# Optimization experiments

Hardware: AMD Instinct MI355X
Metric: run time of the kernel (lower is better)

Reference implementation:

```python
import jax, jax.numpy as jnp
import numpy as np

N_NODES = 50000
N_EDGES = 600000
N_RELS = 19
D_IN = 128
D_HID = 64
D_OUT = 2


def setup_inputs() -> dict:
    key = jax.random.key(0)
    ks = jax.random.split(key, 10)
    feat = jax.random.normal(ks[0], (N_NODES, D_IN), dtype=jnp.float32)
    src = jax.random.randint(ks[1], (N_EDGES,), 0, N_NODES)
    dst = jax.random.randint(ks[2], (N_EDGES,), 0, N_NODES)
    etype = jax.random.randint(ks[3], (N_EDGES,), 0, N_RELS)
    s1 = 1.0 / np.sqrt(D_IN)
    s2 = 1.0 / np.sqrt(D_HID)
    W1 = jax.random.normal(ks[4], (N_RELS, D_IN, D_HID), dtype=jnp.float32) * s1
    loop1 = jax.random.normal(ks[5], (D_IN, D_HID), dtype=jnp.float32) * s1
    b1 = jnp.zeros((D_HID,), dtype=jnp.float32)
    W2 = jax.random.normal(ks[6], (N_RELS, D_HID, D_OUT), dtype=jnp.float32) * s2
    loop2 = jax.random.normal(ks[7], (D_HID, D_OUT), dtype=jnp.float32) * s2
    b2 = jnp.zeros((D_OUT,), dtype=jnp.float32)
    return {"feat": feat, "W1": W1, "loop1": loop1, "b1": b1,
            "W2": W2, "loop2": loop2, "b2": b2,
            "src": src, "dst": dst, "etype": etype}


def _rel_graph_conv(h, W, loop_w, bias, src, dst, etype, activation):
    # Per-relation transform of all nodes: [N, R, O]; then gather per edge.
    # (num_rels * out_feat is small, so this is cheaper than gathering W per edge.)
    transformed = jnp.einsum('nd,rdo->nro', h, W)
    msg = transformed[src, etype]                      # [E, O] edge messages
    agg = jax.ops.segment_sum(msg, dst, num_segments=h.shape[0])  # scatter-add
    out = agg + h @ loop_w + bias                      # self-loop + bias
    if activation is not None:
        out = activation(out)
    return out


def reference(feat, W1, loop1, b1, W2, loop2, b2, src, dst, etype):
    h = _rel_graph_conv(feat, W1, loop1, b1, src, dst, etype, jax.nn.relu)
    h = _rel_graph_conv(h, W2, loop2, b2, src, dst, etype, None)
    return h
```

## Files before the change

kernel.cpp:

```cpp
#include <hip/hip_runtime.h>

#define N_NODES 50000
#define N_EDGES 600000
#define N_RELS  19
#define D_IN    128
#define D_HID   64
#define D_OUT   2
#define BSH     9
#define NB      ((N_NODES + 511) >> 9)
#define NSEG    (NB * N_RELS)
#define SL_BLOCKS ((N_NODES + 63) / 64)
#define PREP_ELEMS (N_RELS * D_HID * D_IN + 64 * 64 + D_HID * D_IN)
#define PREP_BLOCKS ((PREP_ELEMS + 255) / 256)

typedef unsigned short u16;
typedef unsigned int   u32;
typedef __attribute__((ext_vector_type(8))) short sfrag;
typedef __attribute__((ext_vector_type(4))) float f32x4;

__device__ __forceinline__ u16 f2bf(float f){
  union { float f; u32 i; } v; v.f = f;
  u32 r = v.i + 0x7fffu + ((v.i >> 16) & 1u);
  return (u16)(r >> 16);
}
__device__ __forceinline__ float bf2f(u16 u){
  union { u32 i; float f; } v; v.i = ((u32)u) << 16; return v.f;
}
__device__ __forceinline__ u32 pack2(float lo, float hi){
  return (u32)f2bf(lo) | ((u32)f2bf(hi) << 16);
}

__global__ __launch_bounds__(256) void k_pre(const float* __restrict__ feat,
                                             u16* __restrict__ featb,
                                             const int* __restrict__ src,
                                             const int* __restrict__ et,
                                             const int* __restrict__ dst,
                                             int* __restrict__ seg_hist,
                                             int* __restrict__ hist_dst){
  int i = blockIdx.x * 256 + threadIdx.x;
  float4 f = ((const float4*)feat)[i];
  uint2 p; p.x = pack2(f.x, f.y); p.y = pack2(f.z, f.w);
  ((uint2*)featb)[i] = p;
  if (i < N_EDGES) {
    int key = (src[i] >> BSH) * N_RELS + et[i];
    atomicAdd(&seg_hist[key * 16], 1);
    atomicAdd(&hist_dst[dst[i]], 1);
  }
}

__global__ __launch_bounds__(256) void k_prep(
    const int* __restrict__ hist_dst, int* __restrict__ dstart,
    int* __restrict__ cur_dst, int* __restrict__ gcnt,
    const int* __restrict__ seg_hist, int* __restrict__ seg_off,
    int* __restrict__ cur_seg,
    const float* __restrict__ W1, const float* __restrict__ loop1,
    const float* __restrict__ W2, const float* __restrict__ loop2,
    u16* __restrict__ W1Tb, u16* __restrict__ loop1Tb,
    u16* __restrict__ W2allT){
  if (blockIdx.x >= 197) {
    int idx = (blockIdx.x - 197) * 256 + threadIdx.x;
    const int T1  = N_RELS * D_HID * D_IN;
    const int T2c = T1 + 64 * 64;
    const int T3  = T2c + D_HID * D_IN;
    if (idx < T1) {
      int r = idx / (D_HID * D_IN);
      int t = idx - r * (D_HID * D_IN);
      int j = t >> 7, d = t & 127;
      W1Tb[idx] = f2bf(W1[(r * D_IN + d) * D_HID + j]);
    } else if (idx < T2c) {
      int k2 = idx - T1;
      int j = k2 >> 6, k = k2 & 63;
      float val = 0.f;
      if (j < N_RELS * D_OUT)      val = W2[((j >> 1) * D_HID + k) * D_OUT + (j & 1)];
      else if (j == 38)            val = loop2[k * 2];
      else if (j == 39)            val = loop2[k * 2 + 1];
      W2allT[k2] = f2bf(val);
    } else if (idx < T3) {
      int k2 = idx - T2c;
      int j = k2 >> 7, d = k2 & 127;
      loop1Tb[k2] = f2bf(loop1[d * D_HID + j]);
    }
    return;
  }
  if (blockIdx.x == 196) {
    __shared__ int ps[256];
    int tid = threadIdx.x;
    const int PER = (NSEG + 255) / 256;
    int lo = tid * PER, hi = lo + PER; if (hi > NSEG) hi = NSEG; if (lo > NSEG) lo = NSEG;
    int s = 0;
    for (int i = lo; i < hi; ++i) s += seg_hist[i * 16];
    ps[tid] = s;
    __syncthreads();
    if (tid == 0) { int a = 0; for (int j = 0; j < 256; ++j) { int x = ps[j]; ps[j] = a; a += x; } }
    __syncthreads();
    int eo = ps[tid];
    for (int i = lo; i < hi; ++i) {
      int c = seg_hist[i * 16];
      seg_off[i] = eo; cur_seg[i * 16] = eo;
      eo += c;
    }
    if (hi == NSEG) seg_off[NSEG] = eo;
    return;
  }
  __shared__ int wbase[4];
  int tid = threadIdx.x, lane = tid & 63, wv = tid >> 6;
  int n = blockIdx.x * 256 + tid;
  int v = (n < N_NODES) ? hist_dst[n] : 0;
  int x = v;
  #pragma unroll
  for (int o = 1; o < 64; o <<= 1) { int u = __shfl_up(x, o); if (lane >= o) x += u; }
  if (lane == 63) wbase[wv] = atomicAdd(gcnt, x);
  __syncthreads();
  int start = wbase[wv] + x - v;
  if (n < N_NODES) { dstart[n] = start; cur_dst[n] = start; }
}

__global__ __launch_bounds__(256) void k_scatter(const int* __restrict__ src,
                                                 const int* __restrict__ et,
                                                 int* __restrict__ cur_seg,
                                                 int* __restrict__ perm){
  int e = blockIdx.x * 256 + threadIdx.x;
  if (e >= N_EDGES) return;
  int key = (src[e] >> BSH) * N_RELS + et[e];
  int p = atomicAdd(&cur_seg[key * 16], 1);
  perm[p] = e;
}

__global__ __launch_bounds__(256, 4) void k_se1(
    const u16* __restrict__ featb, const u16* __restrict__ W1Tb,
    const u16* __restrict__ loop1Tb, const float* __restrict__ b1,
    const int* __restrict__ src, const int* __restrict__ dst,
    const int* __restrict__ perm, const int* __restrict__ seg_off,
    int* __restrict__ cur_dst, int* __restrict__ srel,
    u16* __restrict__ msgbuf, u16* __restrict__ agg1b){
  __shared__ __align__(16) u16 Bls[64][136];
  __shared__ __align__(16) u16 msg[128][72];
  __shared__ int posIds[128];
  int tid = threadIdx.x, lane = tid & 63, w4 = tid >> 6;
  int r16 = lane & 15, c4 = lane >> 4;

  if (blockIdx.x >= NSEG) {
    int base = (blockIdx.x - NSEG) * 64;
    { int j = tid >> 2, sg = tid & 3;
      const uint4* g = (const uint4*)(loop1Tb + j * 128) + sg * 4;
      uint4* d = (uint4*)&Bls[j][sg * 32];
      d[0] = g[0]; d[1] = g[1]; d[2] = g[2]; d[3] = g[3]; }
    int arow = base + w4 * 16 + r16; if (arow >= N_NODES) arow = N_NODES - 1;
    sfrag aF[4];
    #pragma unroll
    for (int kk = 0; kk < 4; ++kk)
      aF[kk] = *(const sfrag*)(featb + (size_t)arow * D_IN + kk * 32 + c4 * 8);
    __syncthreads();
    #pragma unroll
    for (int ct = 0; ct < 4; ++ct) {
      int col = ct * 16 + r16;
      f32x4 acc = {0.f, 0.f, 0.f, 0.f};
      #pragma unroll
      for (int kk = 0; kk < 4; ++kk) {
        sfrag bF = *(const sfrag*)&Bls[ct * 16 + r16][kk * 32 + c4 * 8];
        acc = __builtin_amdgcn_mfma_f32_16x16x32_bf16(aF[kk], bF, acc, 0, 0, 0);
      }
      float bias = b1[col];
      #pragma unroll
      for (int reg = 0; reg < 4; ++reg) {
        float v = acc[reg] + bias;
        float o = __shfl_xor(v, 1);
        if (!(lane & 1))
          *(u32*)&msg[w4 * 16 + c4 * 4 + reg][col] = pack2(v, o);
      }
    }
    { int j = lane >> 2, q = lane & 3;
      int n = base + w4 * 16 + j;
      if (n < N_NODES) {
        const uint4* mr = (const uint4*)&msg[w4 * 16 + j][q * 16];
        uint4* d = (uint4*)(agg1b + (size_t)n * D_HID + q * 16);
        d[0] = mr[0]; d[1] = mr[1];
      } }
    return;
  }

  const int q8 = NSEG >> 3, r8 = NSEG & 7;
  int xcd = blockIdx.x & 7, cidx = blockIdx.x >> 3;
  int seg = (xcd < r8 ? xcd * (q8 + 1) : r8 * (q8 + 1) + (xcd - r8) * q8) + cidx;
  int ts = seg_off[seg], c = seg_off[seg + 1] - ts;
  if (c == 0) return;
  int rel = seg - (seg / N_RELS) * N_RELS;

  {
    int j = tid >> 2, sg = tid & 3;
    const uint4* g = (const uint4*)(W1Tb + ((size_t)rel * 64 + j) * 128) + sg * 4;
    uint4* d = (uint4*)&Bls[j][sg * 32];
    d[0] = g[0]; d[1] = g[1]; d[2] = g[2]; d[3] = g[3];
  }
  __syncthreads();

  for (int t0 = 0; t0 < c; t0 += 128) {
    int vc = c - t0; if (vc > 128) vc = 128;
    int myPos = -1;
    if (tid < 128 && tid < vc) {
      int e = perm[ts + t0 + tid];
      myPos = atomicAdd(&cur_dst[dst[e]], 1);
      srel[myPos] = (src[e] << 5) | rel;
    }
    sfrag aF[2][4];
    #pragma unroll
    for (int mt = 0; mt < 2; ++mt) {
      int row = w4 * 32 + mt * 16 + r16;
      int rr = row < vc ? row : vc - 1;
      int s = src[perm[ts + t0 + rr]];
      const u16* ap = featb + (size_t)s * D_IN + c4 * 8;
      #pragma unroll
      for (int kk = 0; kk < 4; ++kk)
        aF[mt][kk] = *(const sfrag*)(ap + kk * 32);
    }
    #pragma unroll
    for (int ct = 0; ct < 4; ++ct) {
      sfrag bF[4];
      #pragma unroll
      for (int kk = 0; kk < 4; ++kk)
        bF[kk] = *(const sfrag*)&Bls[ct * 16 + r16][kk * 32 + c4 * 8];
      #pragma unroll
      for (int mt = 0; mt < 2; ++mt) {
        f32x4 acc = {0.f, 0.f, 0.f, 0.f};
        #pragma unroll
        for (int kk = 0; kk < 4; ++kk)
          acc = __builtin_amdgcn_mfma_f32_16x16x32_bf16(aF[mt][kk], bF[kk], acc, 0, 0, 0);
        #pragma unroll
        for (int reg = 0; reg < 4; ++reg) {
          float v = acc[reg];
          float o = __shfl_xor(v, 1);
          if (!(lane & 1)) {
            int orow = w4 * 32 + mt * 16 + c4 * 4 + reg;
            *(u32*)&msg[orow][ct * 16 + r16] = pack2(v, o);
          }
        }
      }
    }
    if (tid < 128) posIds[tid] = myPos;
    __syncthreads();
    { int row = tid >> 1, half = tid & 1;
      int pos = posIds[row];
      if (pos >= 0) {
        const uint4* mr = (const uint4*)&msg[row][half * 32];
        uint4* d = (uint4*)(msgbuf + (size_t)pos * D_HID + half * 32);
        d[0] = mr[0]; d[1] = mr[1]; d[2] = mr[2]; d[3] = mr[3];
      } }
    __syncthreads();
  }
}

__global__ __launch_bounds__(256) void k_agg(
    const u16* __restrict__ msgbuf, const int* __restrict__ dstart,
    const int* __restrict__ cnt, const u16* __restrict__ agg1b,
    const u16* __restrict__ W2allT, const float* __restrict__ b2,
    float* __restrict__ T2f, float* __restrict__ out){
  __shared__ u16   W2ls[64][66];
  __shared__ float h1s[4][68];
  int tid = threadIdx.x, wv = tid >> 6, lane = tid & 63;
  for (int i = tid; i < 64 * 64; i += 256) W2ls[i >> 6][i & 63] = W2allT[i];
  int n = blockIdx.x * 4 + wv;
  int s = dstart[n], epos = s + cnt[n];
  int h = lane >> 5, cc = lane & 31;
  float a0 = 0.f, a1 = 0.f;
  for (int i = s + h; i < epos; i += 2) {
    u32 v = ((const u32*)msgbuf)[(size_t)i * 32 + cc];
    a0 += bf2f((u16)(v & 0xffffu));
    a1 += bf2f((u16)(v >> 16));
  }
  a0 += __shfl_down(a0, 32);
  a1 += __shfl_down(a1, 32);
  if (h == 0) {
    u32 sv = ((const u32*)agg1b)[(size_t)n * 32 + cc];
    float v0 = a0 + bf2f((u16)(sv & 0xffffu));
    float v1 = a1 + bf2f((u16)(sv >> 16));
    v0 = v0 > 0.f ? v0 : 0.f;
    v1 = v1 > 0.f ? v1 : 0.f;
    h1s[wv][2 * cc]     = v0;
    h1s[wv][2 * cc + 1] = v1;
  }
  __syncthreads();
  if (lane < 40) {
    float acc = 0.f;
    #pragma unroll 8
    for (int k = 0; k < 64; ++k)
      acc += bf2f(W2ls[lane][k]) * h1s[wv][k];
    if (lane < 38) T2f[(size_t)n * 40 + lane] = acc;
    else           out[n * 2 + (lane - 38)] = acc + b2[lane - 38];
  }
}

__global__ __launch_bounds__(256) void k_fin(
    const float* __restrict__ T2f, const int* __restrict__ srel,
    const int* __restrict__ dstart, const int* __restrict__ cnt,
    float* __restrict__ out){
  int wv = threadIdx.x >> 6, lane = threadIdx.x & 63;
  int n = blockIdx.x * 4 + wv;
  int s = dstart[n], c = cnt[n];
  float ax = 0.f, ay = 0.f;
  for (int i = lane; i < c; i += 64) {
    int sr = srel[s + i];
    const float* p = T2f + (size_t)(sr >> 5) * 40 + (sr & 31) * 2;
    ax += p[0]; ay += p[1];
  }
  #pragma unroll
  for (int off = 32; off; off >>= 1) {
    ax += __shfl_down(ax, off);
    ay += __shfl_down(ay, off);
  }
  if (lane == 0) {
    out[n * 2]     += ax;
    out[n * 2 + 1] += ay;
  }
}

extern "C" void kernel_launch(void* const* d_in, const int* in_sizes, int n_in,
                              void* d_out, int out_size, void* d_ws, size_t ws_size,
                              hipStream_t stream){
  const float* feat  = (const float*)d_in[0];
  const float* W1    = (const float*)d_in[1];
  const float* loop1 = (const float*)d_in[2];
  const float* b1    = (const float*)d_in[3];
  const float* W2    = (const float*)d_in[4];
  const float* loop2 = (const float*)d_in[5];
  const float* b2    = (const float*)d_in[6];
  const int* src     = (const int*)d_in[7];
  const int* dst     = (const int*)d_in[8];
  const int* et      = (const int*)d_in[9];
  float* out = (float*)d_out;

  char* w = (char*)d_ws;
  u16*   W1Tb     = (u16*)(w);
  u16*   W2allT   = (u16*)(w + 311296);
  u16*   loop1Tb  = (u16*)(w + 319488);
  int*   seg_hist = (int*)(w + 335872);
  int*   gcnt     = (int*)(w + 455040);
  int*   hist_dst = (int*)(w + 455104);
  int*   seg_off  = (int*)(w + 655104);
  int*   cur_seg  = (int*)(w + 662592);
  int*   dstart   = (int*)(w + 781760);
  int*   cur_dst  = (int*)(w + 981760);
  int*   perm     = (int*)(w + 1181760);
  int*   srel     = (int*)(w + 3581760);
  u16*   featb    = (u16*)(w + 5981760);
  float* T2f      = (float*)(w + 5981760);
  u16*   agg1b    = (u16*)(w + 18781760);
  u16*   msgbuf   = (u16*)(w + 25181760);

  hipMemsetAsync(w + 335872, 0, 319232, stream);
  k_pre     <<<6250, 256, 0, stream>>>(feat, featb, src, et, dst, seg_hist, hist_dst);
  k_prep    <<<197 + PREP_BLOCKS, 256, 0, stream>>>(
                hist_dst, dstart, cur_dst, gcnt, seg_hist, seg_off, cur_seg,
                W1, loop1, W2, loop2, W1Tb, loop1Tb, W2allT);
  k_scatter <<<2344, 256, 0, stream>>>(src, et, cur_seg, perm);
  k_se1     <<<NSEG + SL_BLOCKS, 256, 0, stream>>>(
                featb, W1Tb, loop1Tb, b1, src, dst, perm, seg_off,
                cur_dst, srel, msgbuf, agg1b);
  k_agg     <<<12500, 256, 0, stream>>>(msgbuf, dstart, hist_dst, agg1b,
                                        W2allT, b2, T2f, out);
  k_fin     <<<12500, 256, 0, stream>>>(T2f, srel, dstart, hist_dst, out);
}
```

Before: 311.2 us.

## Split edge segments into fixed 128-edge tiles and make final layer edge-parallel atomics

The prep kernel now computes a tile list (segment id and start offset per 128-edge chunk), and the layer-1 message kernel launches one block per tile instead of one block per (node-bucket, relation) segment that looped over its chunks. This is meant to balance load across blocks and expose more parallelism. The final layer-2 aggregation switches from a per-destination-node wave reduction over CSR to an edge-parallel kernel that reads (src,rel,dst) pairs in segment order and does float atomicAdds into the output. The atomic version adds contention and a nondeterministic summation order, and the grid is oversized so many blocks exit early.

```diff
diff --git a/kernel.cpp b/kernel.cpp
--- a/kernel.cpp
+++ b/kernel.cpp
@@ -9,6 +9,7 @@
 #define BSH     9
 #define NB      ((N_NODES + 511) >> 9)
 #define NSEG    (NB * N_RELS)
+#define NTILE_CAP (NSEG + (N_EDGES + 127) / 128)
 #define SL_BLOCKS ((N_NODES + 63) / 64)
 #define PREP_ELEMS (N_RELS * D_HID * D_IN + 64 * 64 + D_HID * D_IN)
 #define PREP_BLOCKS ((PREP_ELEMS + 255) / 256)
@@ -52,7 +53,8 @@
     const int* __restrict__ hist_dst, int* __restrict__ dstart,
     int* __restrict__ cur_dst, int* __restrict__ gcnt,
     const int* __restrict__ seg_hist, int* __restrict__ seg_off,
-    int* __restrict__ cur_seg,
+    int* __restrict__ cur_seg, int* __restrict__ ntile,
+    int* __restrict__ tseg, int* __restrict__ tstart,
     const float* __restrict__ W1, const float* __restrict__ loop1,
     const float* __restrict__ W2, const float* __restrict__ loop2,
     u16* __restrict__ W1Tb, u16* __restrict__ loop1Tb,
@@ -83,21 +85,27 @@
     return;
   }
   if (blockIdx.x == 196) {
-    __shared__ int ps[256];
+    __shared__ int se_s[256], st_s[256];
     int tid = threadIdx.x;
     const int PER = (NSEG + 255) / 256;
     int lo = tid * PER, hi = lo + PER; if (hi > NSEG) hi = NSEG; if (lo > NSEG) lo = NSEG;
-    int s = 0;
-    for (int i = lo; i < hi; ++i) s += seg_hist[i * 16];
-    ps[tid] = s;
+    int se = 0, st = 0;
+    for (int i = lo; i < hi; ++i) { int c = seg_hist[i * 16]; se += c; st += (c + 127) >> 7; }
+    se_s[tid] = se; st_s[tid] = st;
     __syncthreads();
-    if (tid == 0) { int a = 0; for (int j = 0; j < 256; ++j) { int x = ps[j]; ps[j] = a; a += x; } }
+    if (tid == 0) {
+      int a = 0, b = 0;
+      for (int j = 0; j < 256; ++j) { int x = se_s[j], y = st_s[j]; se_s[j] = a; st_s[j] = b; a += x; b += y; }
+      ntile[0] = b;
+    }
     __syncthreads();
-    int eo = ps[tid];
+    int eo = se_s[tid], to = st_s[tid];
     for (int i = lo; i < hi; ++i) {
       int c = seg_hist[i * 16];
       seg_off[i] = eo; cur_seg[i * 16] = eo;
-      eo += c;
+      int nt = (c + 127) >> 7;
+      for (int k = 0; k < nt; ++k) { tseg[to + k] = i; tstart[to + k] = eo + (k << 7); }
+      eo += c; to += nt;
     }
     if (hi == NSEG) seg_off[NSEG] = eo;
     return;
@@ -131,16 +139,18 @@
     const u16* __restrict__ loop1Tb, const float* __restrict__ b1,
     const int* __restrict__ src, const int* __restrict__ dst,
     const int* __restrict__ perm, const int* __restrict__ seg_off,
-    int* __restrict__ cur_dst, int* __restrict__ srel,
-    u16* __restrict__ msgbuf, u16* __restrict__ agg1b){
+    const int* __restrict__ ntile_p, const int* __restrict__ tseg,
+    const int* __restrict__ tstart, int* __restrict__ cur_dst,
+    int2* __restrict__ sd2, u16* __restrict__ msgbuf,
+    u16* __restrict__ agg1b){
   __shared__ __align__(16) u16 Bls[64][136];
   __shared__ __align__(16) u16 msg[128][72];
   __shared__ int posIds[128];
   int tid = threadIdx.x, lane = tid & 63, w4 = tid >> 6;
   int r16 = lane & 15, c4 = lane >> 4;
 
-  if (blockIdx.x >= NSEG) {
-    int base = (blockIdx.x - NSEG) * 64;
+  if (blockIdx.x >= NTILE_CAP) {
+    int base = (blockIdx.x - NTILE_CAP) * 64;
     { int j = tid >> 2, sg = tid & 3;
       const uint4* g = (const uint4*)(loop1Tb + j * 128) + sg * 4;
       uint4* d = (uint4*)&Bls[j][sg * 32];
@@ -179,11 +189,16 @@
     return;
   }
 
-  const int q8 = NSEG >> 3, r8 = NSEG & 7;
-  int xcd = blockIdx.x & 7, cidx = blockIdx.x >> 3;
-  int seg = (xcd < r8 ? xcd * (q8 + 1) : r8 * (q8 + 1) + (xcd - r8) * q8) + cidx;
-  int ts = seg_off[seg], c = seg_off[seg + 1] - ts;
-  if (c == 0) return;
+  int nt = *ntile_p;
+  int pb = blockIdx.x;
+  if (pb >= nt) return;
+  int q8 = nt >> 3, r8 = nt & 7;
+  int xcd = pb & 7, cidx = pb >> 3;
+  int b = (xcd < r8 ? xcd * (q8 + 1) : r8 * (q8 + 1) + (xcd - r8) * q8) + cidx;
+
+  int seg = tseg[b];
+  int ts  = tstart[b];
+  int vc  = seg_off[seg + 1] - ts; if (vc > 128) vc = 128;
   int rel = seg - (seg / N_RELS) * N_RELS;
 
   {
@@ -192,61 +207,57 @@
     uint4* d = (uint4*)&Bls[j][sg * 32];
     d[0] = g[0]; d[1] = g[1]; d[2] = g[2]; d[3] = g[3];
   }
+  int myPos = -1;
+  if (tid < 128 && tid < vc) {
+    int e = perm[ts + tid];
+    int s2 = src[e], d2 = dst[e];
+    myPos = atomicAdd(&cur_dst[d2], 1);
+    sd2[ts + tid] = make_int2((s2 << 5) | rel, d2);
+  }
+  sfrag aF[2][4];
+  #pragma unroll
+  for (int mt = 0; mt < 2; ++mt) {
+    int row = w4 * 32 + mt * 16 + r16;
+    int rr = row < vc ? row : vc - 1;
+    int s = src[perm[ts + rr]];
+    const u16* ap = featb + (size_t)s * D_IN + c4 * 8;
+    #pragma unroll
+    for (int kk = 0; kk < 4; ++kk)
+      aF[mt][kk] = *(const sfrag*)(ap + kk * 32);
+  }
   __syncthreads();
-
-  for (int t0 = 0; t0 < c; t0 += 128) {
-    int vc = c - t0; if (vc > 128) vc = 128;
-    int myPos = -1;
-    if (tid < 128 && tid < vc) {
-      int e = perm[ts + t0 + tid];
-      myPos = atomicAdd(&cur_dst[dst[e]], 1);
-      srel[myPos] = (src[e] << 5) | rel;
-    }
-    sfrag aF[2][4];
+  #pragma unroll
+  for (int ct = 0; ct < 4; ++ct) {
+    sfrag bF[4];
+    #pragma unroll
+    for (int kk = 0; kk < 4; ++kk)
+      bF[kk] = *(const sfrag*)&Bls[ct * 16 + r16][kk * 32 + c4 * 8];
     #pragma unroll
     for (int mt = 0; mt < 2; ++mt) {
-      int row = w4 * 32 + mt * 16 + r16;
-      int rr = row < vc ? row : vc - 1;
-      int s = src[perm[ts + t0 + rr]];
-      const u16* ap = featb + (size_t)s * D_IN + c4 * 8;
+      f32x4 acc = {0.f, 0.f, 0.f, 0.f};
       #pragma unroll
       for (int kk = 0; kk < 4; ++kk)
-        aF[mt][kk] = *(const sfrag*)(ap + kk * 32);
-    }
-    #pragma unroll
-    for (int ct = 0; ct < 4; ++ct) {
-      sfrag bF[4];
+        acc = __builtin_amdgcn_mfma_f32_16x16x32_bf16(aF[mt][kk], bF[kk], acc, 0, 0, 0);
       #pragma unroll
-      for (int kk = 0; kk < 4; ++kk)
-        bF[kk] = *(const sfrag*)&Bls[ct * 16 + r16][kk * 32 + c4 * 8];
-      #pragma unroll
-      for (int mt = 0; mt < 2; ++mt) {
-        f32x4 acc = {0.f, 0.f, 0.f, 0.f};
-        #pragma unroll
-        for (int kk = 0; kk < 4; ++kk)
-          acc = __builtin_amdgcn_mfma_f32_16x16x32_bf16(aF[mt][kk], bF[kk], acc, 0, 0, 0);
-        #pragma unroll
-        for (int reg = 0; reg < 4; ++reg) {
-          float v = acc[reg];
-          float o = __shfl_xor(v, 1);
-          if (!(lane & 1)) {
-            int orow = w4 * 32 + mt * 16 + c4 * 4 + reg;
-            *(u32*)&msg[orow][ct * 16 + r16] = pack2(v, o);
-          }
+      for (int reg = 0; reg < 4; ++reg) {
+        float v = acc[reg];
+        float o = __shfl_xor(v, 1);
+        if (!(lane & 1)) {
+          int orow = w4 * 32 + mt * 16 + c4 * 4 + reg;
+          *(u32*)&msg[orow][ct * 16 + r16] = pack2(v, o);
         }
       }
     }
-    if (tid < 128) posIds[tid] = myPos;
-    __syncthreads();
-    { int row = tid >> 1, half = tid & 1;
-      int pos = posIds[row];
-      if (pos >= 0) {
-        const uint4* mr = (const uint4*)&msg[row][half * 32];
-        uint4* d = (uint4*)(msgbuf + (size_t)pos * D_HID + half * 32);
-        d[0] = mr[0]; d[1] = mr[1]; d[2] = mr[2]; d[3] = mr[3];
-      } }
-    __syncthreads();
-  }
+  }
+  if (tid < 128) posIds[tid] = myPos;
+  __syncthreads();
+  { int row = tid >> 1, half = tid & 1;
+    int pos = posIds[row];
+    if (pos >= 0) {
+      const uint4* mr = (const uint4*)&msg[row][half * 32];
+      uint4* d = (uint4*)(msgbuf + (size_t)pos * D_HID + half * 32);
+      d[0] = mr[0]; d[1] = mr[1]; d[2] = mr[2]; d[3] = mr[3];
+    } }
 }
 
 __global__ __launch_bounds__(256) void k_agg(
@@ -290,27 +301,16 @@
 }
 
 __global__ __launch_bounds__(256) void k_fin(
-    const float* __restrict__ T2f, const int* __restrict__ srel,
-    const int* __restrict__ dstart, const int* __restrict__ cnt,
+    const float* __restrict__ T2f, const int2* __restrict__ sd2,
     float* __restrict__ out){
-  int wv = threadIdx.x >> 6, lane = threadIdx.x & 63;
-  int n = blockIdx.x * 4 + wv;
-  int s = dstart[n], c = cnt[n];
-  float ax = 0.f, ay = 0.f;
-  for (int i = lane; i < c; i += 64) {
-    int sr = srel[s + i];
-    const float* p = T2f + (size_t)(sr >> 5) * 40 + (sr & 31) * 2;
-    ax += p[0]; ay += p[1];
-  }
-  #pragma unroll
-  for (int off = 32; off; off >>= 1) {
-    ax += __shfl_down(ax, off);
-    ay += __shfl_down(ay, off);
-  }
-  if (lane == 0) {
-    out[n * 2]     += ax;
-    out[n * 2 + 1] += ay;
-  }
+  int pb = blockIdx.x;
+  int swz = (pb & 7) * 293 + (pb >> 3);
+  int i = swz * 256 + threadIdx.x;
+  if (i >= N_EDGES) return;
+  int2 v = sd2[i];
+  const float* p = T2f + (size_t)(v.x >> 5) * 40 + (v.x & 31) * 2;
+  atomicAdd(&out[v.y * 2],     p[0]);
+  atomicAdd(&out[v.y * 2 + 1], p[1]);
 }
 
 extern "C" void kernel_launch(void* const* d_in, const int* in_sizes, int n_in,
@@ -337,25 +337,28 @@
   int*   hist_dst = (int*)(w + 455104);
   int*   seg_off  = (int*)(w + 655104);
   int*   cur_seg  = (int*)(w + 662592);
-  int*   dstart   = (int*)(w + 781760);
-  int*   cur_dst  = (int*)(w + 981760);
-  int*   perm     = (int*)(w + 1181760);
-  int*   srel     = (int*)(w + 3581760);
-  u16*   featb    = (u16*)(w + 5981760);
-  float* T2f      = (float*)(w + 5981760);
-  u16*   agg1b    = (u16*)(w + 18781760);
-  u16*   msgbuf   = (u16*)(w + 25181760);
+  int*   ntile    = (int*)(w + 781760);
+  int*   tseg     = (int*)(w + 781824);
+  int*   tstart   = (int*)(w + 808064);
+  int*   dstart   = (int*)(w + 834304);
+  int*   cur_dst  = (int*)(w + 1034304);
+  int*   perm     = (int*)(w + 1234304);
+  int2*  sd2      = (int2*)(w + 3634304);
+  u16*   featb    = (u16*)(w + 8434304);
+  float* T2f      = (float*)(w + 8434304);
+  u16*   agg1b    = (u16*)(w + 21234304);
+  u16*   msgbuf   = (u16*)(w + 27634304);
 
   hipMemsetAsync(w + 335872, 0, 319232, stream);
   k_pre     <<<6250, 256, 0, stream>>>(feat, featb, src, et, dst, seg_hist, hist_dst);
   k_prep    <<<197 + PREP_BLOCKS, 256, 0, stream>>>(
                 hist_dst, dstart, cur_dst, gcnt, seg_hist, seg_off, cur_seg,
-                W1, loop1, W2, loop2, W1Tb, loop1Tb, W2allT);
+                ntile, tseg, tstart, W1, loop1, W2, loop2, W1Tb, loop1Tb, W2allT);
   k_scatter <<<2344, 256, 0, stream>>>(src, et, cur_seg, perm);
-  k_se1     <<<NSEG + SL_BLOCKS, 256, 0, stream>>>(
+  k_se1     <<<NTILE_CAP + SL_BLOCKS, 256, 0, stream>>>(
                 featb, W1Tb, loop1Tb, b1, src, dst, perm, seg_off,
-                cur_dst, srel, msgbuf, agg1b);
+                ntile, tseg, tstart, cur_dst, sd2, msgbuf, agg1b);
   k_agg     <<<12500, 256, 0, stream>>>(msgbuf, dstart, hist_dst, agg1b,
                                         W2allT, b2, T2f, out);
-  k_fin     <<<12500, 256, 0, stream>>>(T2f, srel, dstart, hist_dst, out);
-}
+  k_fin     <<<2344, 256, 0, stream>>>(T2f, sd2, out);
+}
```

Measured after the change: 363.1 us. 16.7% more time.
